# Performance work log

Measured on AMD Instinct MI355X. Metric: run time of the kernel, lower is better.

The kernel has to match this reference:

```python
import jax, jax.numpy as jnp
import numpy as np
import math
from jax import lax

S = 2048   # layer_size (number of neurons)
T = 384    # timesteps per forward call
ALPHA = 0.15
DT = 0.1
THRESH = -50.0
V_RESET = -70.0
VL = -70.0
GL = 0.025
CM = 0.5
TAU = CM / GL                                   # 20.0
COEF = DT ** ALPHA * math.gamma(2.0 - ALPHA) / CM  # dt^alpha * Gamma(2-alpha) / Cm


def setup_inputs() -> dict:
    key = jax.random.key(0)
    I_old = jax.random.normal(key, (S, T), dtype=jnp.float32)
    # class-level fractional (Grunwald-Letnikov style) weight vector, x=5000
    x = 5000
    nv = np.arange(x - 1)
    w = ((x - nv + 1) ** (1.0 - ALPHA) - (x - nv) ** (1.0 - ALPHA)).astype(np.float32)
    return {"I_old": I_old, "weights": jnp.asarray(w)}


def _forward(I_old, weights):
    S_, T_ = I_old.shape
    dtype = I_old.dtype
    # wr[a] = weights[-a]: the memory weight applied to a delta that is `a` steps old.
    # Original: np.inner(weights[-N+1:], delta_trace) pairs oldest delta with weights[-(N-1)]
    # and the newest delta with weights[-1].
    wr = jnp.concatenate([jnp.zeros((1,), dtype), weights[::-1][:T_].astype(dtype)])  # [T+1]
    jidx = jnp.arange(T_)  # buffer slot j holds the delta appended at global step j

    def step(carry, xs):
        V, buf = carry          # V: [S], buf: [S, T] delta history (slot j = delta of step j)
        n, I_n = xs             # n: scalar step index, I_n: [S]
        # fractional memory term: sum_{j=1}^{n-1} wr[n-j] * delta_j
        ages = n - jidx                                        # [T]
        coeff = jnp.where((ages >= 1) & (jidx >= 1),
                          wr[jnp.clip(ages, 0, T_)], jnp.zeros((), dtype))  # [T]
        memory = buf @ coeff                                   # [S]
        # three update rules depending on the global step counter
        V1 = V + (DT / TAU) * (-V + I_n / GL)                  # N == 1 branch
        V2 = COEF * (-GL * (V - VL) + I_n) + V - memory        # N >= 2 branch
        V_pre = jnp.where(n == 0, jnp.full_like(V, -70.0),
                          jnp.where(n == 1, V1, V2))
        spike = (V - THRESH > 0).astype(dtype)                 # spike uses PREVIOUS V
        reset = lax.stop_gradient(spike * (THRESH - V_RESET))  # detached reset
        V_new = V_pre - reset
        buf = buf.at[:, n].set(V_new - V)                      # append delta (n=0 slot masked out)
        return (V_new, buf), (spike, V_new)

    V0 = jnp.zeros((S_,), dtype)          # V_trace initialized to 0 per neuron
    buf0 = jnp.zeros((S_, T_), dtype)
    (_, _), (spk, trc) = lax.scan(step, (V0, buf0), (jnp.arange(T_), I_old.T))
    return spk.T, trc.T                    # each [S, T]


def reference(I_old, weights):
    return _forward(I_old, weights)
```

## Files before the change

kernel.cpp:

```cpp
#include <hip/hip_runtime.h>
#include <cmath>

#define T_STEPS 384
#define CH 64
#define NCH 6
#define WS 392

__device__ __forceinline__ float readlane_f(float v, int l) {
    return __int_as_float(__builtin_amdgcn_readlane(__float_as_int(v), l));
}

__global__ __launch_bounds__(64, 2)
void flif_kernel(const float* __restrict__ I_old, const float* __restrict__ W,
                 float* __restrict__ out, float cm1, float c2, float c3, int Stot)
{
    const int s    = blockIdx.x;
    const int lane = threadIdx.x;

    __shared__ __align__(16) float wrep[4 * WS];
    __shared__ __align__(16) float lrep[4 * 128];
    __shared__ __align__(16) float dbuf[T_STEPS];

    const float* Irow = I_old + (size_t)s * T_STEPS;
    float Inext = Irow[lane];

    #pragma unroll
    for (int r = 0; r < 4; ++r) {
        for (int k = lane; k < WS; k += 64) {
            const int i = k + r;
            wrep[r * WS + k] = (i >= 1 && i <= 383) ? W[4615 + i] : 0.0f;
        }
        for (int k = lane; k < 128; k += 64) {
            const int x = k + r;
            lrep[r * 128 + k] = (x >= 64 && x <= 126) ? W[5062 - x] : 0.0f;
        }
    }
    __syncthreads();

    float wloc[64];
    {
        const int r = lane & 3;
        const float* lp = lrep + r * 128 - r;
        #pragma unroll
        for (int i0 = 0; i0 < 64; i0 += 4) {
            const float4 f = *reinterpret_cast<const float4*>(lp + (lane + 60 - i0));
            wloc[i0 + 0] = f.w; wloc[i0 + 1] = f.z;
            wloc[i0 + 2] = f.y; wloc[i0 + 3] = f.x;
        }
    }

    const int rsel = (-lane) & 3;
    const float* wl = wrep + rsel * WS - lane - rsel;

    float wgt1[64], wgt2[64];
    #pragma unroll
    for (int k = 0; k < 64; k += 4) {
        const float4 f1 = *reinterpret_cast<const float4*>(wl + 320 + k);
        wgt1[k] = f1.x; wgt1[k + 1] = f1.y; wgt1[k + 2] = f1.z; wgt1[k + 3] = f1.w;
        const float4 f2 = *reinterpret_cast<const float4*>(wl + 256 + k);
        wgt2[k] = f2.x; wgt2[k + 1] = f2.y; wgt2[k + 2] = f2.z; wgt2[k + 3] = f2.w;
    }

    float* out_spk = out + (size_t)s * T_STEPS;
    float* out_trc = out + (size_t)Stot * T_STEPS + (size_t)s * T_STEPS;

    const float wr1n = -W[4998];

    float V = 0.0f, d = 0.0f, b = 0.0f, P = 0.0f;

    for (int c = 0; c < NCH; ++c) {
        const int cb = c * CH;
        const float Ic = Inext;
        if (c + 1 < NCH) Inext = Irow[cb + CH + lane];

        float acc = 0.0f;
        for (int cp = 0; cp < c; ++cp) {
            const int g = c - cp;
            const float* dp = dbuf + cp * CH;
            if (g == 1) {
                #pragma unroll
                for (int k = 0; k < 64; k += 4) {
                    const float4 d4 = *reinterpret_cast<const float4*>(dp + k);
                    acc = fmaf(d4.x, wgt1[k],     acc);
                    acc = fmaf(d4.y, wgt1[k + 1], acc);
                    acc = fmaf(d4.z, wgt1[k + 2], acc);
                    acc = fmaf(d4.w, wgt1[k + 3], acc);
                }
            } else if (g == 2) {
                #pragma unroll
                for (int k = 0; k < 64; k += 4) {
                    const float4 d4 = *reinterpret_cast<const float4*>(dp + k);
                    acc = fmaf(d4.x, wgt2[k],     acc);
                    acc = fmaf(d4.y, wgt2[k + 1], acc);
                    acc = fmaf(d4.z, wgt2[k + 2], acc);
                    acc = fmaf(d4.w, wgt2[k + 3], acc);
                }
            } else {
                const float* wp = wl + (384 - 64 * g);
                #pragma unroll
                for (int k = 0; k < 64; k += 4) {
                    const float4 d4 = *reinterpret_cast<const float4*>(dp + k);
                    const float4 w4 = *reinterpret_cast<const float4*>(wp + k);
                    acc = fmaf(d4.x, w4.x, acc);
                    acc = fmaf(d4.y, w4.y, acc);
                    acc = fmaf(d4.z, w4.z, acc);
                    acc = fmaf(d4.w, w4.w, acc);
                }
            }
        }

        float u = fmaf(c3, Ic, c2) - acc;
        const float Vs = V;
        float tc = 0.0f;

        auto body = [&](int i) {
            const float t = fmaf(wr1n, d, P);
            d = t + b;
            P = readlane_f(u, (i + 1) & 63);
            V = V + d;
            const float rv = (V > -50.0f) ? -20.0f : 0.0f;
            b = fmaf(cm1, V, rv);
            u = fmaf(-wloc[i], d, u);
            tc = (lane == i) ? V : tc;
        };

        if (c == 0) {
            V = -90.0f;
            if (lane == 0) tc = V;
            const float I1 = readlane_f(Ic, 1);
            const float V1 = fmaf(0.005f, (I1 / 0.025f) - V, V);
            const float d1 = V1 - V;
            P = readlane_f(u, 2);
            u = fmaf(-wloc[1], d1, u);
            if (lane == 1) tc = V1;
            V = V1;
            d = d1;
            const float rv = (V > -50.0f) ? -20.0f : 0.0f;
            b = fmaf(cm1, V, rv);
            #pragma unroll
            for (int i = 2; i < CH; ++i) body(i);
        } else {
            d = 0.0f;
            P = readlane_f(u, 0);
            #pragma unroll
            for (int i = 0; i < CH; ++i) body(i);
        }

        float prev = __shfl_up(tc, 1);
        if (lane == 0) prev = Vs;
        const float spk = (prev > -50.0f) ? 1.0f : 0.0f;
        float dd = tc - prev;
        if (c == 0 && lane == 0) dd = 0.0f;
        dbuf[cb + lane] = dd;
        out_spk[cb + lane] = spk;
        out_trc[cb + lane] = tc;
    }
}

extern "C" void kernel_launch(void* const* d_in, const int* in_sizes, int n_in,
                              void* d_out, int out_size, void* d_ws, size_t ws_size,
                              hipStream_t stream) {
    const float* I = (const float*)d_in[0];
    const float* W = (const float*)d_in[1];
    float* out = (float*)d_out;
    const int S = in_sizes[0] / T_STEPS;

    const double COEF = std::pow(0.1, 0.15) * std::tgamma(1.85) / 0.5;
    const float c3  = (float)COEF;
    const float cm1 = (float)(-COEF * 0.025);
    const float c2  = (float)(COEF * 0.025 * -70.0);

    flif_kernel<<<S, 64, 0, stream>>>(I, W, out, cm1, c2, c3, S);
}
```

Measured before the change: 85.30 us.

## Overlap far-history memory dot products with the serial recurrence of each chunk

The per-chunk history contributions from chunks two or more steps back are now accumulated for the next chunk inside the serial 64-step recurrence, split into four slices interleaved between groups of 16 steps. Only the adjacent-chunk contribution stays on the critical path before each chunk. This is meant to hide LDS loads and FMAs behind the latency-bound readlane chain. It also drops the wgt2 register array, but fully unrolling the chunk loop increases code size and register pressure.

New measurement: 90.68 us. +6.3%, slower.

```diff
diff --git a/kernel.cpp b/kernel.cpp
--- a/kernel.cpp
+++ b/kernel.cpp
@@ -52,13 +52,11 @@
     const int rsel = (-lane) & 3;
     const float* wl = wrep + rsel * WS - lane - rsel;
 
-    float wgt1[64], wgt2[64];
+    float wgt1[64];
     #pragma unroll
     for (int k = 0; k < 64; k += 4) {
         const float4 f1 = *reinterpret_cast<const float4*>(wl + 320 + k);
         wgt1[k] = f1.x; wgt1[k + 1] = f1.y; wgt1[k + 2] = f1.z; wgt1[k + 3] = f1.w;
-        const float4 f2 = *reinterpret_cast<const float4*>(wl + 256 + k);
-        wgt2[k] = f2.x; wgt2[k + 1] = f2.y; wgt2[k + 2] = f2.z; wgt2[k + 3] = f2.w;
     }
 
     float* out_spk = out + (size_t)s * T_STEPS;
@@ -67,45 +65,25 @@
     const float wr1n = -W[4998];
 
     float V = 0.0f, d = 0.0f, b = 0.0f, P = 0.0f;
+    float accN = 0.0f;
 
+    #pragma unroll
     for (int c = 0; c < NCH; ++c) {
         const int cb = c * CH;
         const float Ic = Inext;
         if (c + 1 < NCH) Inext = Irow[cb + CH + lane];
 
-        float acc = 0.0f;
-        for (int cp = 0; cp < c; ++cp) {
-            const int g = c - cp;
-            const float* dp = dbuf + cp * CH;
-            if (g == 1) {
-                #pragma unroll
-                for (int k = 0; k < 64; k += 4) {
-                    const float4 d4 = *reinterpret_cast<const float4*>(dp + k);
-                    acc = fmaf(d4.x, wgt1[k],     acc);
-                    acc = fmaf(d4.y, wgt1[k + 1], acc);
-                    acc = fmaf(d4.z, wgt1[k + 2], acc);
-                    acc = fmaf(d4.w, wgt1[k + 3], acc);
-                }
-            } else if (g == 2) {
-                #pragma unroll
-                for (int k = 0; k < 64; k += 4) {
-                    const float4 d4 = *reinterpret_cast<const float4*>(dp + k);
-                    acc = fmaf(d4.x, wgt2[k],     acc);
-                    acc = fmaf(d4.y, wgt2[k + 1], acc);
-                    acc = fmaf(d4.z, wgt2[k + 2], acc);
-                    acc = fmaf(d4.w, wgt2[k + 3], acc);
-                }
-            } else {
-                const float* wp = wl + (384 - 64 * g);
-                #pragma unroll
-                for (int k = 0; k < 64; k += 4) {
-                    const float4 d4 = *reinterpret_cast<const float4*>(dp + k);
-                    const float4 w4 = *reinterpret_cast<const float4*>(wp + k);
-                    acc = fmaf(d4.x, w4.x, acc);
-                    acc = fmaf(d4.y, w4.y, acc);
-                    acc = fmaf(d4.z, w4.z, acc);
-                    acc = fmaf(d4.w, w4.w, acc);
-                }
+        float acc = accN;
+        accN = 0.0f;
+        if (c >= 1) {
+            const float* dp = dbuf + (c - 1) * CH;
+            #pragma unroll
+            for (int k = 0; k < 64; k += 4) {
+                const float4 d4 = *reinterpret_cast<const float4*>(dp + k);
+                acc = fmaf(d4.x, wgt1[k],     acc);
+                acc = fmaf(d4.y, wgt1[k + 1], acc);
+                acc = fmaf(d4.z, wgt1[k + 2], acc);
+                acc = fmaf(d4.w, wgt1[k + 3], acc);
             }
         }
 
@@ -124,6 +102,22 @@
             tc = (lane == i) ? V : tc;
         };
 
+        const int nq = (c + 1 < NCH) ? c : 0;
+        auto farq = [&](int q) {
+            #pragma unroll
+            for (int t2 = 0; t2 < nq * 4; ++t2) {
+                const int qi = q * nq * 4 + t2;
+                const int cp = qi >> 4;
+                const int k  = (qi & 15) << 2;
+                const float4 d4 = *reinterpret_cast<const float4*>(dbuf + cp * CH + k);
+                const float4 w4 = *reinterpret_cast<const float4*>(wl + (384 - 64 * (c + 1 - cp)) + k);
+                accN = fmaf(d4.x, w4.x, accN);
+                accN = fmaf(d4.y, w4.y, accN);
+                accN = fmaf(d4.z, w4.z, accN);
+                accN = fmaf(d4.w, w4.w, accN);
+            }
+        };
+
         if (c == 0) {
             V = -90.0f;
             if (lane == 0) tc = V;
@@ -138,12 +132,21 @@
             const float rv = (V > -50.0f) ? -20.0f : 0.0f;
             b = fmaf(cm1, V, rv);
             #pragma unroll
-            for (int i = 2; i < CH; ++i) body(i);
+            for (int i = 2; i < 16; ++i) body(i);
+            #pragma unroll
+            for (int q = 1; q < 4; ++q) {
+                #pragma unroll
+                for (int i = q * 16; i < q * 16 + 16; ++i) body(i);
+            }
         } else {
             d = 0.0f;
             P = readlane_f(u, 0);
             #pragma unroll
-            for (int i = 0; i < CH; ++i) body(i);
+            for (int q = 0; q < 4; ++q) {
+                #pragma unroll
+                for (int i = q * 16; i < q * 16 + 16; ++i) body(i);
+                farq(q);
+            }
         }
 
         float prev = __shfl_up(tc, 1);
```
